# Performance work log

Hardware: AMD Instinct MI355X
Metric: run time of the kernel (lower is better)

The kernel has to match this reference:

```python
import jax, jax.numpy as jnp
import numpy as np

_L, _DEPTH, _M, _NGEN, _C = 4, 7, 256, 8, 16


def _build_tree():
    # Complete _L-ary tree in BFS (level) order. t columns: [label, parent, position, child_0.._L-1]
    rng = np.random.default_rng(0)
    sizes = [_L ** d for d in range(_DEPTH + 1)]
    t_limits = np.concatenate([[0], np.cumsum(sizes)]).astype(np.int32)
    n = int(t_limits[-1])
    u = np.arange(n)
    parent = np.where(u > 0, (u - 1) // _L, 0)
    pos = np.where(u > 0, (u - 1) % _L, 0)
    labels = rng.integers(0, _M, n)
    ch = _L * u[:, None] + 1 + np.arange(_L)[None, :]
    ch = np.where(ch < n, ch, 0)  # 0 == no child (root is never a child)
    t = np.concatenate([labels[:, None], parent[:, None], pos[:, None], ch], axis=1).astype(np.int32)
    return t, t_limits


def setup_inputs():
    key = jax.random.key(0)
    ka, kb, kp = jax.random.split(key, 3)
    t, t_limits = _build_tree()
    return {
        'a': jax.random.normal(ka, (_NGEN, _C, _C, _L), jnp.float32),
        'b': jax.random.normal(kb, (_NGEN, _C, _M), jnp.float32),
        'pi': jax.random.normal(kp, (_NGEN, _C), jnp.float32),
        't': jnp.asarray(t),
        't_limits': jnp.asarray(t_limits),
    }


def _htmm_likelihood(a, b, pi, t, t_limits):
    t = np.asarray(t)
    lim = np.asarray(t_limits)
    n_levels = len(lim) - 1
    n = int(lim[-1])
    n_gen, C, _, L = a.shape
    sm_a = jax.nn.softmax(a, axis=1)    # [G, Ci(child), Cj(parent), L]
    sm_b = jax.nn.softmax(b, axis=2)    # [G, C, M]
    sm_pi = jax.nn.softmax(pi, axis=1)  # [G, C]

    # ---- preliminary downward: per-node state priors, level by level ----
    prior = jnp.zeros((n_gen, n, C), sm_pi.dtype).at[:, 0, :].set(sm_pi)
    for lev in range(1, n_levels):
        lo, hi = int(lim[lev]), int(lim[lev + 1])
        pos, pa = t[lo:hi, 2], t[lo:hi, 1]
        a_pos = sm_a[:, :, :, pos]                        # [G, Ci, Cj, nl]
        lev_prior = jnp.einsum('gijn,gnj->gni', a_pos, prior[:, pa, :])
        prior = prior.at[:, lo:hi, :].set(lev_prior)

    # ---- upward pass ----
    beta_i = jnp.zeros((n_gen, n, C), sm_pi.dtype)
    beta_il = jnp.zeros((n_gen, n + 1, C), sm_pi.dtype)   # extra dummy slot for padded children
    lo, hi = int(lim[-2]), int(lim[-1])                   # leaves
    em = sm_b[:, :, t[lo:hi, 0]].transpose(0, 2, 1)       # [G, n_leaf, C]
    bl = em * prior[:, lo:hi, :]
    beta_i = beta_i.at[:, lo:hi, :].set(bl / bl.sum(2, keepdims=True))
    a_t = sm_a.transpose(0, 3, 1, 2)                      # [G, L(pos), Ci, Cj]
    for lev in range(n_levels - 2, -1, -1):
        lo, hi = int(lim[lev]), int(lim[lev + 1])
        ch = t[lo:hi, 3:]                                 # [nl, L]
        mask = ch > 0
        safe = np.where(mask, ch, 0)
        ratio = beta_i[:, safe, :] / prior[:, safe, :]    # [G, nl, L, C]
        bil = jnp.einsum('gnlc,glcp->gnlp', ratio, a_t)   # [G, nl, L, Cj]
        aux = jnp.prod(jnp.where(mask[None, :, :, None], bil, 1.0), axis=2)
        em = sm_b[:, :, t[lo:hi, 0]].transpose(0, 2, 1)
        bi = aux * em * prior[:, lo:hi, :]
        beta_i = beta_i.at[:, lo:hi, :].set(bi / bi.sum(2, keepdims=True))
        scat = np.where(mask, ch, n).reshape(-1)          # padded children go to dummy slot
        beta_il = beta_il.at[:, scat, :].set(bil.reshape(n_gen, -1, C))
    beta_il = beta_il[:, :n, :].at[:, 0, :].set(0.0)

    # ---- downward pass: smoothed posteriors ----
    eps_i = jnp.zeros((n_gen, n, C), sm_pi.dtype).at[:, 0, :].set(beta_i[:, 0, :])
    eps_ijl = jnp.zeros((n_gen, n, C, C), sm_pi.dtype)
    for lev in range(1, n_levels):
        lo, hi = int(lim[lev]), int(lim[lev + 1])
        pos, pa = t[lo:hi, 2], t[lo:hi, 1]
        a_pos = sm_a[:, :, :, pos].transpose(0, 3, 1, 2)  # [G, nl, Ci, Cj]
        num = beta_i[:, lo:hi, :, None] * a_pos * eps_i[:, pa, None, :]
        den = prior[:, lo:hi, :, None] * beta_il[:, lo:hi, None, :]
        e_ijl = num / den
        e_i = e_ijl.sum(3)
        e_i = e_i / e_i.sum(2, keepdims=True)
        eps_i = eps_i.at[:, lo:hi, :].set(e_i)
        eps_ijl = eps_ijl.at[:, lo:hi, :, :].set(e_ijl)

    # ---- log-likelihood ----
    pi_lh = jnp.sum(eps_i[:, 0, :] * jnp.log(sm_pi), axis=-1)
    b_nodes = sm_b[:, :, t[:, 0]].transpose(0, 2, 1)      # [G, n, C]
    b_lh = jnp.sum(eps_i * jnp.log(b_nodes), axis=(1, 2))
    a_pos_all = sm_a[:, :, :, t[1:, 2]].transpose(0, 3, 1, 2)
    a_lh = jnp.sum(eps_ijl[:, 1:] * jnp.log(a_pos_all), axis=(1, 2, 3))
    return pi_lh + b_lh + a_lh  # [n_gen]


def reference(a, b, pi, t, t_limits):
    return _htmm_likelihood(a, b, pi, t, t_limits)
```

## Files before the change

### kernel.cpp

```cpp
#include <hip/hip_runtime.h>

#define NGEN 8
#define NC 16
#define NM 256

#define OFF_SMA_T  ((size_t)0)
#define OFF_SALA   ((size_t)8192)
#define OFF_SMA_U  ((size_t)16384)
#define OFF_SMB_T  ((size_t)24576)
#define OFF_LSMB_T ((size_t)57344)
#define OFF_SMPI   ((size_t)90112)
#define OFF_LSMPI  ((size_t)90240)
#define OFF_R4     ((size_t)112224)
#define OFF_EPS4   ((size_t)144992)
#define OFF_PT     ((size_t)177760)
#define OFF_ST     ((size_t)221424)
#define ST_R7   0
#define ST_R6   1024
#define ST_R5   1280
#define ST_BIL7 1344
#define ST_BIL6 2368
#define ST_BIL5 2624
#define ST_LAB  2688
#define ST_SZ   2784

template <int CTRL>
__device__ __forceinline__ float dpp_row_add(float v) {
    int s = __builtin_amdgcn_update_dpp(0, __float_as_int(v), CTRL, 0xf, 0xf, false);
    return v + __int_as_float(s);
}
__device__ __forceinline__ float red16(float v) {
    v = dpp_row_add<0x121>(v);
    v = dpp_row_add<0x122>(v);
    v = dpp_row_add<0x124>(v);
    v = dpp_row_add<0x128>(v);
    return v;
}
__device__ __forceinline__ float rcpf(float x) { return __builtin_amdgcn_rcpf(x); }

__device__ __forceinline__ float dot16(const float* A, const float* row) {
    const float4* r4 = (const float4*)row;
    float s = 0.f;
#pragma unroll
    for (int q = 0; q < 4; ++q) {
        float4 rr = r4[q];
        s += A[4 * q] * rr.x + A[4 * q + 1] * rr.y + A[4 * q + 2] * rr.z + A[4 * q + 3] * rr.w;
    }
    return s;
}
__device__ __forceinline__ void dot16x2(const float* A, const float* B, const float* row,
                                        float& s1, float& s2) {
    const float4* r4 = (const float4*)row;
#pragma unroll
    for (int q = 0; q < 4; ++q) {
        float4 rr = r4[q];
        s1 += A[4 * q] * rr.x + A[4 * q + 1] * rr.y + A[4 * q + 2] * rr.z + A[4 * q + 3] * rr.w;
        s2 += B[4 * q] * rr.x + B[4 * q + 1] * rr.y + B[4 * q + 2] * rr.z + B[4 * q + 3] * rr.w;
    }
}

__device__ __forceinline__ void up_step4(const float (*Rch)[16], float (*BILch)[16],
                                         const float (*Ppar)[16], float (*Rpar)[16],
                                         const float* smb, int lab, int nd, int l, int p,
                                         const float* Aup) {
    int ch = 4 * nd + l;
    float bil = dot16(Aup, Rch[ch]);
    BILch[ch][p] = bil;
    float t0 = bil * __shfl_xor(bil, 16);
    float aux = t0 * __shfl_xor(t0, 32);
    float q0 = aux * smb[(size_t)lab * 16 + p];
    float bi = q0 * Ppar[nd][p];
    float ssum = red16(bi);
    if (l == 0) Rpar[nd][p] = q0 * rcpf(ssum);
}

__global__ __launch_bounds__(256) void k_init(const float* __restrict__ a,
                                              const float* __restrict__ b,
                                              const float* __restrict__ pi,
                                              float* __restrict__ ws, float* __restrict__ out) {
    int bx = blockIdx.x, tid = threadIdx.x;
    __shared__ __align__(16) float sAs[1024];
    __shared__ __align__(16) float P[341][16];
    if (bx < 128) {
        if (tid < 64) {
            int g = bx >> 4, i = bx & 15;
            float v[4];
            float mx = -1e30f;
#pragma unroll
            for (int q = 0; q < 4; ++q) {
                v[q] = b[((size_t)(g * NC + i)) * NM + tid + 64 * q];
                mx = fmaxf(mx, v[q]);
            }
#pragma unroll
            for (int o = 1; o < 64; o <<= 1) mx = fmaxf(mx, __shfl_xor(mx, o));
            float e[4], s = 0.f;
#pragma unroll
            for (int q = 0; q < 4; ++q) { e[q] = expf(v[q] - mx); s += e[q]; }
#pragma unroll
            for (int o = 1; o < 64; o <<= 1) s += __shfl_xor(s, o);
            float ls = logf(s), rs = 1.0f / s;
#pragma unroll
            for (int q = 0; q < 4; ++q) {
                int m = tid + 64 * q;
                ws[OFF_SMB_T + ((size_t)g * NM + m) * NC + i] = e[q] * rs;
                ws[OFF_LSMB_T + ((size_t)g * NM + m) * NC + i] = v[q] - mx - ls;
            }
        }
        return;
    }
    int g = bx - 128;
    if (tid < 64) {
        int j = tid >> 2, l = tid & 3;
        size_t base = ((size_t)(g * NC) * NC + j) * 4 + l;
        float v[16];
        float mx = -1e30f;
#pragma unroll
        for (int i = 0; i < 16; ++i) { v[i] = a[base + (size_t)i * 64]; mx = fmaxf(mx, v[i]); }
        float e[16], s = 0.0f;
#pragma unroll
        for (int i = 0; i < 16; ++i) { e[i] = expf(v[i] - mx); s += e[i]; }
        float ls = logf(s), rs = 1.0f / s;
        size_t tb = ((size_t)(g * NC + j) * 4 + l) * NC;
#pragma unroll
        for (int i = 0; i < 16; ++i) {
            float sm = e[i] * rs;
            float lg = v[i] - mx - ls;
            ws[OFF_SMA_T + tb + i] = sm;
            ws[OFF_SALA + tb + i] = sm * lg;
            ws[OFF_SMA_U + ((size_t)(g * NC + i) * 4 + l) * NC + j] = sm;
            sAs[(j * 4 + l) * 16 + i] = sm;
        }
    } else if (tid == 64) {
        float v[16];
        float mx = -1e30f;
#pragma unroll
        for (int i = 0; i < 16; ++i) { v[i] = pi[g * NC + i]; mx = fmaxf(mx, v[i]); }
        float e[16], s = 0.0f;
#pragma unroll
        for (int i = 0; i < 16; ++i) { e[i] = expf(v[i] - mx); s += e[i]; }
        float ls = logf(s), rs = 1.0f / s;
#pragma unroll
        for (int i = 0; i < 16; ++i) {
            float sm = e[i] * rs;
            ws[OFF_SMPI + g * NC + i] = sm;
            ws[OFF_LSMPI + g * NC + i] = v[i] - mx - ls;
            P[0][i] = sm;
        }
        out[g] = 0.0f;
    }
    __syncthreads();
    int i = tid & 15, grp = tid >> 4, pos = grp & 3;
    float Areg[16];
#pragma unroll
    for (int j = 0; j < 16; ++j) Areg[j] = sAs[(j * 4 + pos) * 16 + i];
    if (grp < 4) P[1 + grp][i] = dot16(Areg, P[0]);
    __syncthreads();
    P[5 + grp][i] = dot16(Areg, P[1 + (grp >> 2)]);
    __syncthreads();
#pragma unroll
    for (int k = 0; k < 4; ++k) {
        int nl = grp + 16 * k;
        P[21 + nl][i] = dot16(Areg, P[5 + (nl >> 2)]);
    }
    __syncthreads();
#pragma unroll
    for (int k = 0; k < 16; ++k) {
        int nl = grp + 16 * k;
        P[85 + nl][i] = dot16(Areg, P[21 + (nl >> 2)]);
    }
    __syncthreads();
    float* dst = ws + OFF_PT + (size_t)g * 341 * 16;
    for (int k = tid; k < 341 * 4; k += 256) ((float4*)dst)[k] = ((const float4*)&P[0][0])[k];
}

__global__ __launch_bounds__(256) void k_sub_up(float* __restrict__ ws,
                                                const int* __restrict__ t) {
    int s = blockIdx.x, g = blockIdx.y, tid = threadIdx.x;
    int v = 85 + s;
    int i = tid & 15, grp = tid >> 4, pos = grp & 3;
    int lane = tid & 63, wv = tid >> 6;
    int l = lane >> 4, p = lane & 15;
    const float* sAg = ws + OFF_SMA_T + (size_t)g * 1024;
    const float* Aug = ws + OFF_SMA_U + (size_t)g * 1024;
    const float* smb = ws + OFF_SMB_T + (size_t)g * 4096;
    const float* ptg = ws + OFF_PT + (size_t)g * 341 * 16;

    __shared__ __align__(16) float ST[ST_SZ];
    float (*R7)[16]   = (float(*)[16])(ST + ST_R7);
    float (*R6)[16]   = (float(*)[16])(ST + ST_R6);
    float (*R5)[16]   = (float(*)[16])(ST + ST_R5);
    float (*BIL7)[16] = (float(*)[16])(ST + ST_BIL7);
    float (*BIL6)[16] = (float(*)[16])(ST + ST_BIL6);
    float (*BIL5)[16] = (float(*)[16])(ST + ST_BIL5);
    int* labs = (int*)(ST + ST_LAB);
    __shared__ __align__(16) float P5[4][16], P6[16][16];
    __shared__ __align__(16) float P4[16];

    if (tid < 64) labs[21 + tid] = t[(64 * v + 21 + tid) * 7];
    else if (tid < 80) labs[5 + (tid - 64)] = t[(16 * v + 5 + (tid - 64)) * 7];
    else if (tid < 84) labs[1 + (tid - 80)] = t[(4 * v + 1 + (tid - 80)) * 7];
    else if (tid == 84) labs[0] = t[v * 7];
    else if (tid >= 96 && tid < 112) P4[tid - 96] = ptg[(size_t)(85 + s) * 16 + (tid - 96)];
    float Areg[16];
#pragma unroll
    for (int j = 0; j < 16; ++j) Areg[j] = sAg[(j * 4 + pos) * 16 + i];
    __syncthreads();

    if (tid < 64) P5[grp][i] = dot16(Areg, P4);
    __syncthreads();
    P6[grp][i] = dot16(Areg, P5[grp >> 2]);
    __syncthreads();
#pragma unroll
    for (int k = 0; k < 4; ++k) {
        int nl = grp + 16 * k;
        float s7 = dot16(Areg, P6[nl >> 2]);
        float smbv = smb[(size_t)labs[21 + nl] * 16 + i];
        float bl = smbv * s7;
        float ssum = red16(bl);
        R7[nl][i] = smbv * rcpf(ssum);
    }
    __syncthreads();
    float Aup[16];
#pragma unroll
    for (int c = 0; c < 16; ++c) Aup[c] = Aug[(c * 4 + l) * 16 + p];
#pragma unroll
    for (int r = 0; r < 4; ++r)
        up_step4(R7, BIL7, P6, R6, smb, labs[5 + (wv + 4 * r)], wv + 4 * r, l, p, Aup);
    __syncthreads();
    up_step4(R6, BIL6, P5, R5, smb, labs[1 + wv], wv, l, p, Aup);
    __syncthreads();
    if (wv == 0) {
        float bil = dot16(Aup, R5[l]);
        BIL5[l][p] = bil;
        float t0 = bil * __shfl_xor(bil, 16);
        float aux = t0 * __shfl_xor(t0, 32);
        float q0 = aux * smb[(size_t)labs[0] * 16 + p];
        float bi = q0 * P4[p];
        float ssum = red16(bi);
        if (l == 0) ws[OFF_R4 + ((size_t)g * 256 + s) * 16 + p] = q0 * rcpf(ssum);
    }
    __syncthreads();
    float* dst = ws + OFF_ST + (size_t)(g * 256 + s) * ST_SZ;
    for (int k = tid; k < ST_SZ / 4; k += 256) ((float4*)dst)[k] = ((const float4*)ST)[k];
}

__global__ __launch_bounds__(1024) void k_top(float* __restrict__ ws, const int* __restrict__ t,
                                              float* __restrict__ out) {
    int g = blockIdx.x, tid = threadIdx.x;
    int i = tid & 15, grp = tid >> 4, pos = grp & 3;
    int lane = tid & 63, wv = tid >> 6;
    int l = lane >> 4, p = lane & 15;
    const float* sAg = ws + OFF_SMA_T + (size_t)g * 1024;
    const float* sLg = ws + OFF_SALA + (size_t)g * 1024;
    const float* Aug = ws + OFF_SMA_U + (size_t)g * 1024;
    const float* smb = ws + OFF_SMB_T + (size_t)g * 4096;
    const float* lsmb = ws + OFF_LSMB_T + (size_t)g * 4096;
    const float* ptg = ws + OFF_PT + (size_t)g * 341 * 16;
    const float* r4g = ws + OFF_R4 + (size_t)g * 4096;
    float* eps4 = ws + OFF_EPS4 + (size_t)g * 4096;

    __shared__ __align__(16) float Pt[85][16], Bt[85][16], BILt[341][16];
    __shared__ int labt[341];
    __shared__ float wsum[16];

    float Areg[16], Aup[16], sLreg[16];
#pragma unroll
    for (int j = 0; j < 16; ++j) {
        Areg[j] = sAg[(j * 4 + pos) * 16 + i];
        sLreg[j] = sLg[(j * 4 + pos) * 16 + i];
    }
#pragma unroll
    for (int c = 0; c < 16; ++c) Aup[c] = Aug[(c * 4 + l) * 16 + p];
    for (int k = tid; k < 85 * 4; k += 1024) ((float4*)&Pt[0][0])[k] = ((const float4*)ptg)[k];
    if (tid < 341) labt[tid] = t[tid * 7];
    __syncthreads();
    for (int r = 0; r < 4; ++r) {
        int nd = wv + 16 * r;
        int chl = 4 * nd + l;
        float rv = r4g[(size_t)chl * 16 + p];
        float bil = 0.f;
#pragma unroll
        for (int c = 0; c < 16; ++c) bil += __shfl(rv, c, 16) * Aup[c];
        BILt[85 + chl][p] = bil;
        float t0 = bil * __shfl_xor(bil, 16);
        float aux = t0 * __shfl_xor(t0, 32);
        float bi = aux * smb[(size_t)labt[21 + nd] * 16 + p] * Pt[21 + nd][p];
        float ssum = red16(bi);
        if (l == 0) Bt[21 + nd][p] = bi * rcpf(ssum);
    }
    __syncthreads();
    {
        int nd = wv, ch = 21 + 4 * nd + l;
        float rv = Bt[ch][p] * rcpf(Pt[ch][p]);
        float bil = 0.f;
#pragma unroll
        for (int c = 0; c < 16; ++c) bil += __shfl(rv, c, 16) * Aup[c];
        BILt[ch][p] = bil;
        float t0 = bil * __shfl_xor(bil, 16);
        float aux = t0 * __shfl_xor(t0, 32);
        float bi = aux * smb[(size_t)labt[5 + nd] * 16 + p] * Pt[5 + nd][p];
        float ssum = red16(bi);
        if (l == 0) Bt[5 + nd][p] = bi * rcpf(ssum);
    }
    __syncthreads();
    if (wv < 4) {
        int nd = wv, ch = 5 + 4 * nd + l;
        float rv = Bt[ch][p] * rcpf(Pt[ch][p]);
        float bil = 0.f;
#pragma unroll
        for (int c = 0; c < 16; ++c) bil += __shfl(rv, c, 16) * Aup[c];
        BILt[ch][p] = bil;
        float t0 = bil * __shfl_xor(bil, 16);
        float aux = t0 * __shfl_xor(t0, 32);
        float bi = aux * smb[(size_t)labt[1 + nd] * 16 + p] * Pt[1 + nd][p];
        float ssum = red16(bi);
        if (l == 0) Bt[1 + nd][p] = bi * rcpf(ssum);
    }
    __syncthreads();
    if (wv == 0) {
        int ch = 1 + l;
        float rv = Bt[ch][p] * rcpf(Pt[ch][p]);
        float bil = 0.f;
#pragma unroll
        for (int c = 0; c < 16; ++c) bil += __shfl(rv, c, 16) * Aup[c];
        BILt[ch][p] = bil;
        float t0 = bil * __shfl_xor(bil, 16);
        float aux = t0 * __shfl_xor(t0, 32);
        float bi = aux * smb[(size_t)labt[0] * 16 + p] * Pt[0][p];
        float ssum = red16(bi);
        if (l == 0) Bt[0][p] = bi * rcpf(ssum);
    }
    __syncthreads();
    float acc = 0.f;
    if (tid < 16)
        acc += Bt[0][i] * (ws[OFF_LSMPI + g * 16 + i] + lsmb[(size_t)labt[0] * 16 + i]);
    if (grp < 4) {
        int row = 1 + grp;
        float w = Bt[0][i] * rcpf(BILt[row][i]);
        BILt[row][i] = w;
        float c0 = Bt[row][i] * rcpf(Pt[row][i]);
        float s1 = 0.f, s2 = 0.f;
        dot16x2(Areg, sLreg, BILt[row], s1, s2);
        float esum = c0 * s1, tot = red16(esum), ev = esum * rcpf(tot);
        Bt[row][i] = ev;
        acc += c0 * s2 + ev * lsmb[(size_t)labt[row] * 16 + i];
    }
    __syncthreads();
    if (grp < 16) {
        int row = 5 + grp;
        float w = Bt[1 + (grp >> 2)][i] * rcpf(BILt[row][i]);
        BILt[row][i] = w;
        float c0 = Bt[row][i] * rcpf(Pt[row][i]);
        float s1 = 0.f, s2 = 0.f;
        dot16x2(Areg, sLreg, BILt[row], s1, s2);
        float esum = c0 * s1, tot = red16(esum), ev = esum * rcpf(tot);
        Bt[row][i] = ev;
        acc += c0 * s2 + ev * lsmb[(size_t)labt[row] * 16 + i];
    }
    __syncthreads();
    {
        int row = 21 + grp;
        float w = Bt[5 + (grp >> 2)][i] * rcpf(BILt[row][i]);
        BILt[row][i] = w;
        float c0 = Bt[row][i] * rcpf(Pt[row][i]);
        float s1 = 0.f, s2 = 0.f;
        dot16x2(Areg, sLreg, BILt[row], s1, s2);
        float esum = c0 * s1, tot = red16(esum), ev = esum * rcpf(tot);
        Bt[row][i] = ev;
        acc += c0 * s2 + ev * lsmb[(size_t)labt[row] * 16 + i];
    }
    __syncthreads();
    for (int k = 0; k < 4; ++k) {
        int nl = grp + 64 * k;
        int row = 85 + nl;
        float w = Bt[21 + (nl >> 2)][i] * rcpf(BILt[row][i]);
        BILt[row][i] = w;
        float c0 = r4g[(size_t)nl * 16 + i];
        float s1 = 0.f, s2 = 0.f;
        dot16x2(Areg, sLreg, BILt[row], s1, s2);
        float esum = c0 * s1, tot = red16(esum), ev = esum * rcpf(tot);
        eps4[(size_t)nl * 16 + i] = ev;
        acc += c0 * s2 + ev * lsmb[(size_t)labt[row] * 16 + i];
    }
#pragma unroll
    for (int o = 1; o < 64; o <<= 1) acc += __shfl_xor(acc, o);
    if ((tid & 63) == 0) wsum[tid >> 6] = acc;
    __syncthreads();
    if (tid == 0) {
        float stot = 0.f;
#pragma unroll
        for (int w2 = 0; w2 < 16; ++w2) stot += wsum[w2];
        atomicAdd(&out[g], stot);
    }
}

__global__ __launch_bounds__(256) void k_sub_down(float* __restrict__ ws, float* __restrict__ out) {
    int s = blockIdx.x, g = blockIdx.y, tid = threadIdx.x;
    int i = tid & 15, grp = tid >> 4, pos = grp & 3;
    const float* sAg = ws + OFF_SMA_T + (size_t)g * 1024;
    const float* sLg = ws + OFF_SALA + (size_t)g * 1024;
    const float* lsmb = ws + OFF_LSMB_T + (size_t)g * 4096;

    __shared__ __align__(16) float ST[ST_SZ];
    float (*R7)[16]   = (float(*)[16])(ST + ST_R7);
    float (*R6)[16]   = (float(*)[16])(ST + ST_R6);
    float (*R5)[16]   = (float(*)[16])(ST + ST_R5);
    float (*BIL7)[16] = (float(*)[16])(ST + ST_BIL7);
    float (*BIL6)[16] = (float(*)[16])(ST + ST_BIL6);
    float (*BIL5)[16] = (float(*)[16])(ST + ST_BIL5);
    const int* labs = (const int*)(ST + ST_LAB);
    __shared__ __align__(16) float E4[16];
    __shared__ float wsum[4];

    const float* src = ws + OFF_ST + (size_t)(g * 256 + s) * ST_SZ;
    for (int k = tid; k < ST_SZ / 4; k += 256) ((float4*)ST)[k] = ((const float4*)src)[k];
    if (tid >= 96 && tid < 112)
        E4[tid - 96] = ws[OFF_EPS4 + ((size_t)g * 256 + s) * 16 + (tid - 96)];

    float Areg[16], sLreg[16];
#pragma unroll
    for (int j = 0; j < 16; ++j) {
        Areg[j] = sAg[(j * 4 + pos) * 16 + i];
        sLreg[j] = sLg[(j * 4 + pos) * 16 + i];
    }
    __syncthreads();

    float acc = 0.f;
    if (tid < 64) {
        float w = E4[i] * rcpf(BIL5[grp][i]);
        BIL5[grp][i] = w;
        float c0 = R5[grp][i];
        float s1 = 0.f, s2 = 0.f;
        dot16x2(Areg, sLreg, BIL5[grp], s1, s2);
        float esum = c0 * s1, tot = red16(esum), ev = esum * rcpf(tot);
        R5[grp][i] = ev;
        acc += c0 * s2 + ev * lsmb[(size_t)labs[1 + grp] * 16 + i];
    }
    __syncthreads();
    {
        float w = R5[grp >> 2][i] * rcpf(BIL6[grp][i]);
        BIL6[grp][i] = w;
        float c0 = R6[grp][i];
        float s1 = 0.f, s2 = 0.f;
        dot16x2(Areg, sLreg, BIL6[grp], s1, s2);
        float esum = c0 * s1, tot = red16(esum), ev = esum * rcpf(tot);
        R6[grp][i] = ev;
        acc += c0 * s2 + ev * lsmb[(size_t)labs[5 + grp] * 16 + i];
    }
    __syncthreads();
#pragma unroll
    for (int k = 0; k < 4; ++k) {
        int nl = grp + 16 * k;
        float w = R6[nl >> 2][i] * rcpf(BIL7[nl][i]);
        BIL7[nl][i] = w;
        float c0 = R7[nl][i];
        float s1 = 0.f, s2 = 0.f;
        dot16x2(Areg, sLreg, BIL7[nl], s1, s2);
        float esum = c0 * s1, tot = red16(esum), ev = esum * rcpf(tot);
        acc += c0 * s2 + ev * lsmb[(size_t)labs[21 + nl] * 16 + i];
    }
#pragma unroll
    for (int o = 1; o < 64; o <<= 1) acc += __shfl_xor(acc, o);
    if ((tid & 63) == 0) wsum[tid >> 6] = acc;
    __syncthreads();
    if (tid == 0) atomicAdd(&out[g], wsum[0] + wsum[1] + wsum[2] + wsum[3]);
}

extern "C" void kernel_launch(void* const* d_in, const int* in_sizes, int n_in,
                              void* d_out, int out_size, void* d_ws, size_t ws_size,
                              hipStream_t stream) {
    const float* a = (const float*)d_in[0];
    const float* b = (const float*)d_in[1];
    const float* pi = (const float*)d_in[2];
    const int* t = (const int*)d_in[3];
    float* out = (float*)d_out;
    float* ws = (float*)d_ws;

    k_init<<<136, 256, 0, stream>>>(a, b, pi, ws, out);
    k_sub_up<<<dim3(256, NGEN), 256, 0, stream>>>(ws, t);
    k_top<<<NGEN, 1024, 0, stream>>>(ws, t, out);
    k_sub_down<<<dim3(256, NGEN), 256, 0, stream>>>(ws, out);
}
```

Before: 65.01 us.

## Move level-4 downward step from single-block top kernel into per-subtree kernels

The top kernel (one block per generator) no longer processes the 256 level-4 nodes. It writes level-3 posteriors instead. Each subtree block now computes its own level-4 node's posterior from the parent's eps, its precomputed child-beta (stored by the upward kernel) and its R4. This shrinks the serial, low-parallelism top kernel and spreads the work across 2048 blocks, at the cost of an extra sync and a few extra global loads per subtree block.

Result: no change. 63.95 us (-1.6%).

```diff
diff --git a/kernel.cpp b/kernel.cpp
--- a/kernel.cpp
+++ b/kernel.cpp
@@ -12,9 +12,10 @@
 #define OFF_SMPI   ((size_t)90112)
 #define OFF_LSMPI  ((size_t)90240)
 #define OFF_R4     ((size_t)112224)
-#define OFF_EPS4   ((size_t)144992)
+#define OFF_BIL4   ((size_t)144992)
 #define OFF_PT     ((size_t)177760)
-#define OFF_ST     ((size_t)221424)
+#define OFF_EPS3   ((size_t)221408)
+#define OFF_ST     ((size_t)229600)
 #define ST_R7   0
 #define ST_R6   1024
 #define ST_R5   1280
@@ -237,7 +238,15 @@
         float q0 = aux * smb[(size_t)labs[0] * 16 + p];
         float bi = q0 * P4[p];
         float ssum = red16(bi);
-        if (l == 0) ws[OFF_R4 + ((size_t)g * 256 + s) * 16 + p] = q0 * rcpf(ssum);
+        float r4v = q0 * rcpf(ssum);
+        if (l == 0) {
+            ws[OFF_R4 + ((size_t)g * 256 + s) * 16 + p] = r4v;
+            P4[p] = r4v;
+        }
+        if (l == (s & 3)) {
+            float bil4 = dot16(Aup, P4);
+            ws[OFF_BIL4 + ((size_t)g * 256 + s) * 16 + p] = bil4;
+        }
     }
     __syncthreads();
     float* dst = ws + OFF_ST + (size_t)(g * 256 + s) * ST_SZ;
@@ -257,10 +266,10 @@
     const float* lsmb = ws + OFF_LSMB_T + (size_t)g * 4096;
     const float* ptg = ws + OFF_PT + (size_t)g * 341 * 16;
     const float* r4g = ws + OFF_R4 + (size_t)g * 4096;
-    float* eps4 = ws + OFF_EPS4 + (size_t)g * 4096;
-
-    __shared__ __align__(16) float Pt[85][16], Bt[85][16], BILt[341][16];
-    __shared__ int labt[341];
+    float* eps3 = ws + OFF_EPS3 + (size_t)g * 1024;
+
+    __shared__ __align__(16) float Pt[85][16], Bt[85][16], BILt[85][16];
+    __shared__ int labt[85];
     __shared__ float wsum[16];
 
     float Areg[16], Aup[16], sLreg[16];
@@ -272,7 +281,7 @@
 #pragma unroll
     for (int c = 0; c < 16; ++c) Aup[c] = Aug[(c * 4 + l) * 16 + p];
     for (int k = tid; k < 85 * 4; k += 1024) ((float4*)&Pt[0][0])[k] = ((const float4*)ptg)[k];
-    if (tid < 341) labt[tid] = t[tid * 7];
+    if (tid < 85) labt[tid] = t[tid * 7];
     __syncthreads();
     for (int r = 0; r < 4; ++r) {
         int nd = wv + 16 * r;
@@ -281,7 +290,6 @@
         float bil = 0.f;
 #pragma unroll
         for (int c = 0; c < 16; ++c) bil += __shfl(rv, c, 16) * Aup[c];
-        BILt[85 + chl][p] = bil;
         float t0 = bil * __shfl_xor(bil, 16);
         float aux = t0 * __shfl_xor(t0, 32);
         float bi = aux * smb[(size_t)labt[21 + nd] * 16 + p] * Pt[21 + nd][p];
@@ -366,20 +374,7 @@
         float s1 = 0.f, s2 = 0.f;
         dot16x2(Areg, sLreg, BILt[row], s1, s2);
         float esum = c0 * s1, tot = red16(esum), ev = esum * rcpf(tot);
-        Bt[row][i] = ev;
-        acc += c0 * s2 + ev * lsmb[(size_t)labt[row] * 16 + i];
-    }
-    __syncthreads();
-    for (int k = 0; k < 4; ++k) {
-        int nl = grp + 64 * k;
-        int row = 85 + nl;
-        float w = Bt[21 + (nl >> 2)][i] * rcpf(BILt[row][i]);
-        BILt[row][i] = w;
-        float c0 = r4g[(size_t)nl * 16 + i];
-        float s1 = 0.f, s2 = 0.f;
-        dot16x2(Areg, sLreg, BILt[row], s1, s2);
-        float esum = c0 * s1, tot = red16(esum), ev = esum * rcpf(tot);
-        eps4[(size_t)nl * 16 + i] = ev;
+        eps3[(size_t)grp * 16 + i] = ev;
         acc += c0 * s2 + ev * lsmb[(size_t)labt[row] * 16 + i];
     }
 #pragma unroll
@@ -409,13 +404,17 @@
     float (*BIL6)[16] = (float(*)[16])(ST + ST_BIL6);
     float (*BIL5)[16] = (float(*)[16])(ST + ST_BIL5);
     const int* labs = (const int*)(ST + ST_LAB);
-    __shared__ __align__(16) float E4[16];
+    __shared__ __align__(16) float E3[16], B4r[16], R4r[16], W4[16], E4[16];
     __shared__ float wsum[4];
 
     const float* src = ws + OFF_ST + (size_t)(g * 256 + s) * ST_SZ;
     for (int k = tid; k < ST_SZ / 4; k += 256) ((float4*)ST)[k] = ((const float4*)src)[k];
     if (tid >= 96 && tid < 112)
-        E4[tid - 96] = ws[OFF_EPS4 + ((size_t)g * 256 + s) * 16 + (tid - 96)];
+        E3[tid - 96] = ws[OFF_EPS3 + ((size_t)g * 64 + (s >> 2)) * 16 + (tid - 96)];
+    else if (tid >= 112 && tid < 128)
+        B4r[tid - 112] = ws[OFF_BIL4 + ((size_t)g * 256 + s) * 16 + (tid - 112)];
+    else if (tid >= 192 && tid < 208)
+        R4r[tid - 192] = ws[OFF_R4 + ((size_t)g * 256 + s) * 16 + (tid - 192)];
 
     float Areg[16], sLreg[16];
 #pragma unroll
@@ -426,6 +425,17 @@
     __syncthreads();
 
     float acc = 0.f;
+    if (grp == (s & 3)) {
+        float w = E3[i] * rcpf(B4r[i]);
+        W4[i] = w;
+        float c0 = R4r[i];
+        float s1 = 0.f, s2 = 0.f;
+        dot16x2(Areg, sLreg, W4, s1, s2);
+        float esum = c0 * s1, tot = red16(esum), ev = esum * rcpf(tot);
+        E4[i] = ev;
+        acc += c0 * s2 + ev * lsmb[(size_t)labs[0] * 16 + i];
+    }
+    __syncthreads();
     if (tid < 64) {
         float w = E4[i] * rcpf(BIL5[grp][i]);
         BIL5[grp][i] = w;
```
